# Performance work log

Hardware: AMD Instinct MI355X
Metric: run time of the kernel (lower is better)

Reference implementation:

```python
import jax, jax.numpy as jnp
import numpy as np

D_MODEL = 1024
D_STATE = 16
D_CONV = 4
EXPAND = 2
HEADDIM = 8
D_INNER = EXPAND * D_MODEL            # 2048
NHEADS = D_INNER // HEADDIM           # 256
CONV_DIM = D_INNER + 2 * D_STATE      # 2080 (ngroups=1)
D_IN_PROJ = 2 * D_INNER + 2 * D_STATE + NHEADS  # 4384
B_SZ, SEQ = 4, 2048
EPS = 1e-5


def setup_inputs() -> dict:
    key = jax.random.key(0)
    ks = jax.random.split(key, 8)
    return {
        "x": jax.random.normal(ks[0], (B_SZ, SEQ, D_MODEL), jnp.float32),
        "ln_w": jnp.ones((D_MODEL,), jnp.float32),
        "ln_b": jnp.zeros((D_MODEL,), jnp.float32),
        "W_in": jax.random.normal(ks[1], (D_MODEL, D_IN_PROJ), jnp.float32) * 0.02,
        "conv_w": jax.random.normal(ks[2], (D_CONV, 1, CONV_DIM), jnp.float32) * 0.2,
        "conv_b": jnp.zeros((CONV_DIM,), jnp.float32),
        "A_log": jnp.log(jax.random.uniform(ks[3], (NHEADS,), jnp.float32, 1.0, 16.0)),
        "Dp": jnp.ones((NHEADS,), jnp.float32) + 0.1 * jax.random.normal(ks[4], (NHEADS,), jnp.float32),
        "dt_bias": 0.5 * jax.random.normal(ks[5], (NHEADS,), jnp.float32),
        "rms_w": jnp.ones((D_INNER,), jnp.float32),
        "W_out": jax.random.normal(ks[6], (D_INNER, D_MODEL), jnp.float32) * 0.02,
    }


def _mamba_block(x, ln_w, ln_b, W_in, conv_w, conv_b, A_log, Dp, dt_bias, rms_w, W_out):
    B, L, _ = x.shape
    # pre-norm LayerNorm
    mu = jnp.mean(x, axis=-1, keepdims=True)
    var = jnp.mean((x - mu) ** 2, axis=-1, keepdims=True)
    xn = (x - mu) * jax.lax.rsqrt(var + EPS) * ln_w + ln_b

    # in_proj -> z, xBC, dt
    u = xn @ W_in                                    # (B, L, 4384)
    z = u[..., :D_INNER]
    xBC = u[..., D_INNER:D_INNER + CONV_DIM]
    dt = jax.nn.softplus(u[..., -NHEADS:] + dt_bias)  # (B, L, NHEADS)

    # causal depthwise conv1d + SiLU
    xp = jnp.pad(xBC, ((0, 0), (D_CONV - 1, 0), (0, 0)))
    xBC = jax.lax.conv_general_dilated(
        xp, conv_w, window_strides=(1,), padding="VALID",
        dimension_numbers=("NWC", "WIO", "NWC"), feature_group_count=CONV_DIM)
    xBC = jax.nn.silu(xBC + conv_b)

    xs = xBC[..., :D_INNER].reshape(B, L, NHEADS, HEADDIM)   # SSM input
    Bm = xBC[..., D_INNER:D_INNER + D_STATE]                  # (B, L, N)
    Cm = xBC[..., D_INNER + D_STATE:]                          # (B, L, N)

    A = -jnp.exp(A_log)                                       # (NHEADS,)

    def step(h, inp):
        # h: (B, H, P, N)
        x_t, B_t, C_t, dt_t = inp
        dA = jnp.exp(dt_t * A)                                 # (B, H)
        h = h * dA[..., None, None] + jnp.einsum("bh,bhp,bn->bhpn", dt_t, x_t, B_t)
        y = jnp.einsum("bhpn,bn->bhp", h, C_t)
        return h, y

    h0 = jnp.zeros((B, NHEADS, HEADDIM, D_STATE), x.dtype)
    _, ys = jax.lax.scan(step, h0, (xs.swapaxes(0, 1), Bm.swapaxes(0, 1),
                                     Cm.swapaxes(0, 1), dt.swapaxes(0, 1)))
    y = ys.swapaxes(0, 1) + Dp[None, None, :, None] * xs       # (B, L, H, P)
    y = y.reshape(B, L, D_INNER)

    # gated RMSNorm: rmsnorm(y * silu(z)) * weight
    g = y * jax.nn.silu(z)
    g = g * jax.lax.rsqrt(jnp.mean(g * g, axis=-1, keepdims=True) + EPS) * rms_w

    return x + g @ W_out


def reference(x, ln_w, ln_b, W_in, conv_w, conv_b, A_log, Dp, dt_bias, rms_w, W_out):
    return _mamba_block(x, ln_w, ln_b, W_in, conv_w, conv_b, A_log, Dp, dt_bias, rms_w, W_out)
```

## Files before the change

### kernel.cpp

```cpp
#include <hip/hip_runtime.h>

typedef __bf16 bf16;
typedef __attribute__((ext_vector_type(8))) __bf16 bf16x8;
typedef __attribute__((ext_vector_type(4))) float f32x4;

#define B_SZ 4
#define SEQ 2048
#define DM 1024
#define DIN 2048
#define NH 256
#define DSTATE 16
#define CONVD 2080
#define DPROJ 4384
#define NPAD1 4608
#define MROWS 8192
#define NC 64
#define LC 32
#define UROWB 8768

__device__ __forceinline__ void gload_lds16(const void* g, void* l) {
  __builtin_amdgcn_global_load_lds(
      (__attribute__((address_space(1))) void*)g,
      (__attribute__((address_space(3))) void*)l, 16, 0, 0);
}

template <int N>
__device__ __forceinline__ void vm_wait() {
  asm volatile("s_waitcnt vmcnt(%0)" ::"n"(N) : "memory");
}
__device__ __forceinline__ void bar() { asm volatile("s_barrier" ::: "memory"); }
__device__ __forceinline__ void lgkm0() {
  asm volatile("s_waitcnt lgkmcnt(0)" ::: "memory");
}

__global__ void transpose_cvt(const float* __restrict__ W, bf16* __restrict__ WT,
                              int K, int N, int Npad) {
  __shared__ float tile[32][33];
  int k0 = blockIdx.x * 32, n0 = blockIdx.y * 32;
  int tx = threadIdx.x, ty = threadIdx.y;
#pragma unroll
  for (int j = 0; j < 4; j++) {
    int k = k0 + ty + 8 * j, n = n0 + tx;
    tile[ty + 8 * j][tx] = (k < K && n < N) ? W[(size_t)k * N + n] : 0.f;
  }
  __syncthreads();
#pragma unroll
  for (int j = 0; j < 4; j++) {
    int n = n0 + ty + 8 * j, k = k0 + tx;
    if (n < Npad && k < K) WT[(size_t)n * K + k] = (bf16)tile[tx][ty + 8 * j];
  }
}

__global__ __launch_bounds__(256) void ln_kernel(const float* __restrict__ x,
                                                 const float* __restrict__ lw,
                                                 const float* __restrict__ lb,
                                                 bf16* __restrict__ xn) {
  int row = blockIdx.x;
  int t = threadIdx.x;
  f32x4 v4 = ((const f32x4*)(x + (size_t)row * DM))[t];
  float v0 = v4[0], v1 = v4[1], v2 = v4[2], v3 = v4[3];
  float s = v0 + v1 + v2 + v3;
  float s2 = v0 * v0 + v1 * v1 + v2 * v2 + v3 * v3;
#pragma unroll
  for (int off = 32; off > 0; off >>= 1) {
    s += __shfl_down(s, off);
    s2 += __shfl_down(s2, off);
  }
  __shared__ float ps[8];
  int wave = t >> 6, lane = t & 63;
  if (lane == 0) { ps[wave] = s; ps[4 + wave] = s2; }
  __syncthreads();
  s = ps[0] + ps[1] + ps[2] + ps[3];
  s2 = ps[4] + ps[5] + ps[6] + ps[7];
  float mean = s * (1.f / DM);
  float var = s2 * (1.f / DM) - mean * mean;
  float rstd = rsqrtf(var + 1e-5f);
  f32x4 wv = ((const f32x4*)lw)[t];
  f32x4 bv = ((const f32x4*)lb)[t];
  bf16 o[4];
  o[0] = (bf16)((v0 - mean) * rstd * wv[0] + bv[0]);
  o[1] = (bf16)((v1 - mean) * rstd * wv[1] + bv[1]);
  o[2] = (bf16)((v2 - mean) * rstd * wv[2] + bv[2]);
  o[3] = (bf16)((v3 - mean) * rstd * wv[3] + bv[3]);
  bf16* dst = xn + (size_t)row * DM + t * 4;
  dst[0] = o[0]; dst[1] = o[1]; dst[2] = o[2]; dst[3] = o[3];
}

#define G1_PHASE(MQ, NQ, P, STAGE, VMW)                                                    \
  {                                                                                        \
    const char* sa_ = lds + ((P) * 2 + (MQ)) * 16384;                                      \
    const char* sb_ = lds + 65536 + ((P) * 2 + (NQ)) * 16384;                              \
    bf16x8 a_[4][2], b_[2][2];                                                             \
    _Pragma("unroll") for (int mi = 0; mi < 4; mi++) {                                     \
      int lrow = wm * 64 + mi * 16 + lr16;                                                 \
      a_[mi][0] = *(const bf16x8*)(sa_ + lrow * 128 + ts0 * 16);                           \
      a_[mi][1] = *(const bf16x8*)(sa_ + lrow * 128 + ts1 * 16);                           \
    }                                                                                      \
    _Pragma("unroll") for (int ni = 0; ni < 2; ni++) {                                     \
      int lrow = wn * 32 + ni * 16 + lr16;                                                 \
      b_[ni][0] = *(const bf16x8*)(sb_ + lrow * 128 + ts0 * 16);                           \
      b_[ni][1] = *(const bf16x8*)(sb_ + lrow * 128 + ts1 * 16);                           \
    }                                                                                      \
    STAGE;                                                                                 \
    VMW;                                                                                   \
    bar();                                                                                 \
    lgkm0();                                                                               \
    __builtin_amdgcn_s_setprio(1);                                                         \
    _Pragma("unroll") for (int mi = 0; mi < 4; mi++)                                       \
      _Pragma("unroll") for (int ni = 0; ni < 2; ni++) {                                   \
        acc[(MQ) * 4 + mi][(NQ) * 2 + ni] = __builtin_amdgcn_mfma_f32_16x16x32_bf16(       \
            a_[mi][0], b_[ni][0], acc[(MQ) * 4 + mi][(NQ) * 2 + ni], 0, 0, 0);             \
        acc[(MQ) * 4 + mi][(NQ) * 2 + ni] = __builtin_amdgcn_mfma_f32_16x16x32_bf16(       \
            a_[mi][1], b_[ni][1], acc[(MQ) * 4 + mi][(NQ) * 2 + ni], 0, 0, 0);             \
      }                                                                                    \
    __builtin_amdgcn_s_setprio(0);                                                         \
    bar();                                                                                 \
  }

__global__ __launch_bounds__(512, 2) void gemm1_8p(const bf16* __restrict__ A,
                                                   const bf16* __restrict__ BT,
                                                   bf16* __restrict__ C) {
  __shared__ char lds[131072];
  int bid = blockIdx.x;
  int swz = (bid & 7) * 72 + (bid >> 3);
  int bm = swz / 18, bn = swz - (swz / 18) * 18;
  int m0 = bm * 256, n0 = bn * 256;
  int t = threadIdx.x, lane = t & 63, wave = t >> 6;
  int wm = wave >> 2, wn = wave & 3;
  int lr16 = lane & 15, kq = lane >> 4;
  int ts0 = kq ^ (lr16 & 7);
  int ts1 = (4 + kq) ^ (lr16 & 7);
  int sw = (lane & 7) ^ ((lane >> 3) & 7);
  int l8 = lane >> 3;
  int c0 = 2 * wave, c1 = 2 * wave + 1;
  int lr0 = c0 * 8 + l8, lr1 = c1 * 8 + l8;
  const char* Ab = (const char*)A;
  const char* Bb = (const char*)BT;
  int grA0 = m0 + (lr0 >> 6) * 128 + (lr0 & 63);
  int grA1 = m0 + (lr1 >> 6) * 128 + (lr1 & 63);
  int gcB0 = n0 + (lr0 >> 5) * 64 + (lr0 & 31);
  int gcB1 = n0 + (lr1 >> 5) * 64 + (lr1 & 31);

  auto stA = [&](int kt, int p, int mq) {
    char* slot = lds + (p * 2 + mq) * 16384;
    size_t ko = (size_t)kt * 128 + sw * 16;
    gload_lds16(Ab + (size_t)(grA0 + mq * 64) * 2048 + ko, slot + c0 * 1024);
    gload_lds16(Ab + (size_t)(grA1 + mq * 64) * 2048 + ko, slot + c1 * 1024);
  };
  auto stB = [&](int kt, int p, int nq) {
    char* slot = lds + 65536 + (p * 2 + nq) * 16384;
    size_t ko = (size_t)kt * 128 + sw * 16;
    gload_lds16(Bb + (size_t)(gcB0 + nq * 32) * 2048 + ko, slot + c0 * 1024);
    gload_lds16(Bb + (size_t)(gcB1 + nq * 32) * 2048 + ko, slot + c1 * 1024);
  };

  f32x4 acc[8][4] = {};
  stA(0, 0, 0); stB(0, 0, 0); stA(0, 0, 1); stB(0, 0, 1); stA(1, 1, 0); stB(1, 1, 0);
  vm_wait<8>();
  bar();
#pragma unroll 1
  for (int kt = 0; kt < 16; kt++) {
    int p = kt & 1;
    G1_PHASE(0, 0, p, { if (kt + 1 < 16) stA(kt + 1, p ^ 1, 1); },
             { if (kt < 15) vm_wait<6>(); else vm_wait<0>(); });
    G1_PHASE(0, 1, p, { if (kt + 1 < 16) stB(kt + 1, p ^ 1, 1); }, {});
    G1_PHASE(1, 0, p, { if (kt + 2 < 16) stA(kt + 2, p, 0); }, {});
    G1_PHASE(1, 1, p, { if (kt + 2 < 16) stB(kt + 2, p, 0); },
             { if (kt < 14) vm_wait<8>(); else if (kt == 14) vm_wait<4>(); });
  }
#pragma unroll
  for (int mq = 0; mq < 2; mq++)
#pragma unroll
    for (int mi = 0; mi < 4; mi++)
#pragma unroll
      for (int nq = 0; nq < 2; nq++)
#pragma unroll
        for (int ni = 0; ni < 2; ni++) {
          int row = m0 + wm * 128 + mq * 64 + mi * 16 + kq * 4;
          int col = n0 + wn * 64 + nq * 32 + ni * 16 + lr16;
          f32x4 v = acc[mq * 4 + mi][nq * 2 + ni];
          if (col < 4384) {
#pragma unroll
            for (int r = 0; r < 4; r++)
              C[(size_t)(row + r) * DPROJ + col] = (bf16)v[r];
          }
        }
}

#define G2_PHASE(MQ, P, STAGE, VMW)                                                        \
  {                                                                                        \
    const char* sa_ = lds + ((P) * 2 + (MQ)) * 16384;                                      \
    const char* sb_ = lds + 65536 + (P) * 16384;                                           \
    bf16x8 a_[4][2], b_[2][2];                                                             \
    _Pragma("unroll") for (int mi = 0; mi < 4; mi++) {                                     \
      int lrow = wm * 64 + mi * 16 + lr16;                                                 \
      a_[mi][0] = *(const bf16x8*)(sa_ + lrow * 128 + ts0 * 16);                           \
      a_[mi][1] = *(const bf16x8*)(sa_ + lrow * 128 + ts1 * 16);                           \
    }                                                                                      \
    _Pragma("unroll") for (int ni = 0; ni < 2; ni++) {                                     \
      int lrow = wn * 32 + ni * 16 + lr16;                                                 \
      b_[ni][0] = *(const bf16x8*)(sb_ + lrow * 128 + ts0 * 16);                           \
      b_[ni][1] = *(const bf16x8*)(sb_ + lrow * 128 + ts1 * 16);                           \
    }                                                                                      \
    STAGE;                                                                                 \
    VMW;                                                                                   \
    bar();                                                                                 \
    lgkm0();                                                                               \
    __builtin_amdgcn_s_setprio(1);                                                         \
    _Pragma("unroll") for (int mi = 0; mi < 4; mi++)                                       \
      _Pragma("unroll") for (int ni = 0; ni < 2; ni++) {                                   \
        acc[(MQ) * 4 + mi][ni] = __builtin_amdgcn_mfma_f32_16x16x32_bf16(                  \
            a_[mi][0], b_[ni][0], acc[(MQ) * 4 + mi][ni], 0, 0, 0);                        \
        acc[(MQ) * 4 + mi][ni] = __builtin_amdgcn_mfma_f32_16x16x32_bf16(                  \
            a_[mi][1], b_[ni][1], acc[(MQ) * 4 + mi][ni], 0, 0, 0);                        \
      }                                                                                    \
    __builtin_amdgcn_s_setprio(0);                                                         \
    bar();                                                                                 \
  }

__global__ __launch_bounds__(512, 2) void gemm2_8p(const bf16* __restrict__ A,
                                                   const bf16* __restrict__ BT,
                                                   float* __restrict__ C,
                                                   const float* __restrict__ Xres) {
  __shared__ char lds[98304];
  int bid = blockIdx.x;
  int swz = (bid & 7) * 32 + (bid >> 3);
  int bm = swz >> 3, bn = swz & 7;
  int m0 = bm * 256, n0 = bn * 128;
  int t = threadIdx.x, lane = t & 63, wave = t >> 6;
  int wm = wave >> 2, wn = wave & 3;
  int lr16 = lane & 15, kq = lane >> 4;
  int ts0 = kq ^ (lr16 & 7);
  int ts1 = (4 + kq) ^ (lr16 & 7);
  int sw = (lane & 7) ^ ((lane >> 3) & 7);
  int l8 = lane >> 3;
  int c0 = 2 * wave, c1 = 2 * wave + 1;
  int lr0 = c0 * 8 + l8, lr1 = c1 * 8 + l8;
  const char* Ab = (const char*)A;
  const char* Bb = (const char*)BT;
  int grA0 = m0 + (lr0 >> 6) * 128 + (lr0 & 63);
  int grA1 = m0 + (lr1 >> 6) * 128 + (lr1 & 63);
  int gcB0 = n0 + lr0, gcB1 = n0 + lr1;

  auto stA = [&](int kt, int p, int mq) {
    char* slot = lds + (p * 2 + mq) * 16384;
    size_t ko = (size_t)kt * 128 + sw * 16;
    gload_lds16(Ab + (size_t)(grA0 + mq * 64) * 4096 + ko, slot + c0 * 1024);
    gload_lds16(Ab + (size_t)(grA1 + mq * 64) * 4096 + ko, slot + c1 * 1024);
  };
  auto stB = [&](int kt, int p) {
    char* slot = lds + 65536 + p * 16384;
    size_t ko = (size_t)kt * 128 + sw * 16;
    gload_lds16(Bb + (size_t)gcB0 * 4096 + ko, slot + c0 * 1024);
    gload_lds16(Bb + (size_t)gcB1 * 4096 + ko, slot + c1 * 1024);
  };

  f32x4 acc[8][2] = {};
  stA(0, 0, 0); stB(0, 0); stA(0, 0, 1); stA(1, 1, 0);
  vm_wait<4>();
  bar();
#pragma unroll 1
  for (int kt = 0; kt < 32; kt++) {
    int p = kt & 1;
    G2_PHASE(0, p, { if (kt + 1 < 32) { stB(kt + 1, p ^ 1); stA(kt + 1, p ^ 1, 1); } },
             { if (kt < 31) vm_wait<6>(); else vm_wait<0>(); });
    G2_PHASE(1, p, { if (kt + 2 < 32) stA(kt + 2, p, 0); },
             { if (kt < 30) vm_wait<4>(); else if (kt == 30) vm_wait<2>(); });
  }
#pragma unroll
  for (int mq = 0; mq < 2; mq++)
#pragma unroll
    for (int mi = 0; mi < 4; mi++)
#pragma unroll
      for (int ni = 0; ni < 2; ni++) {
        int row = m0 + wm * 128 + mq * 64 + mi * 16 + kq * 4;
        int col = n0 + wn * 32 + ni * 16 + lr16;
        f32x4 v = acc[mq * 4 + mi][ni];
#pragma unroll
        for (int r = 0; r < 4; r++) {
          size_t o = (size_t)(row + r) * DM + col;
          C[o] = Xres[o] + v[r];
        }
      }
}

__global__ __launch_bounds__(256) void conv_prep3(const bf16* __restrict__ u,
                                                  const float* __restrict__ cw,
                                                  const float* __restrict__ cb,
                                                  const float* __restrict__ dt_bias,
                                                  bf16* __restrict__ xs,
                                                  float* __restrict__ BC,
                                                  float* __restrict__ dtf) {
  const int JPR = 292;
  int idx = blockIdx.x * 256 + threadIdx.x;
  if (idx >= MROWS * JPR) return;
  int row = idx / JPR;
  int j = idx - row * JPR;
  int t = row & (SEQ - 1);
  if (j < 260) {
    int c0 = j * 8;
    float acc[8];
#pragma unroll
    for (int i = 0; i < 8; i++) acc[i] = cb[c0 + i];
    const bf16* ub = u + (size_t)row * DPROJ + DIN + c0;
#pragma unroll
    for (int tap = 0; tap < 4; tap++) {
      int tt = t - 3 + tap;
      if (tt >= 0) {
        bf16x8 uv = *(const bf16x8*)(ub + (ptrdiff_t)(tap - 3) * DPROJ);
        const float* wv = cw + tap * CONVD + c0;
#pragma unroll
        for (int i = 0; i < 8; i++) acc[i] += wv[i] * (float)uv[i];
      }
    }
    if (c0 < DIN) {
      bf16x8 o;
#pragma unroll
      for (int i = 0; i < 8; i++) {
        float sv = acc[i] / (1.f + __expf(-acc[i]));
        o[i] = (bf16)sv;
      }
      *(bf16x8*)(xs + (size_t)row * DIN + c0) = o;
    } else {
      float* bc = BC + (size_t)row * 32 + (c0 - DIN);
#pragma unroll
      for (int i = 0; i < 8; i++) bc[i] = acc[i] / (1.f + __expf(-acc[i]));
    }
  } else {
    int h0 = (j - 260) * 8;
    bf16x8 uv = *(const bf16x8*)(u + (size_t)row * DPROJ + (DPROJ - NH) + h0);
    float* dst = dtf + (size_t)row * NH + h0;
#pragma unroll
    for (int i = 0; i < 8; i++) {
      float xv = (float)uv[i] + dt_bias[h0 + i];
      dst[i] = (xv > 20.f) ? xv : log1pf(__expf(xv));
    }
  }
}

__global__ __launch_bounds__(64) void scan_p1(const bf16* __restrict__ xs,
                                              const float* __restrict__ BC,
                                              const float* __restrict__ dtf,
                                              const float* __restrict__ A_log,
                                              bf16* __restrict__ uscr) {
  int c = blockIdx.x & 63, hg = (blockIdx.x >> 6) & 31, b = blockIdx.x >> 11;
  int lane = threadIdx.x, hh = lane >> 3;
  int h = hg * 8 + hh;
  float A = -__expf(A_log[h]);
  float st[16];
#pragma unroll
  for (int n = 0; n < 16; n++) st[n] = 0.f;
  float pcum = 1.f;
  size_t rb = (size_t)b * SEQ + (size_t)c * LC;
  for (int t = 0; t < LC; t++) {
    size_t row = rb + t;
    const float* bcrow = BC + row * 32;
    float dtv = dtf[row * NH + h];
    float x = (float)xs[row * DIN + hg * 64 + lane];
    float dA = __expf(dtv * A);
    pcum *= dA;
    float w = dtv * x;
#pragma unroll
    for (int n = 0; n < 16; n++) st[n] = st[n] * dA + w * bcrow[n];
  }
  char* slot = (char*)uscr + (size_t)blockIdx.x * UROWB + 4096;
  float* S = (float*)slot;
#pragma unroll
  for (int n = 0; n < 16; n++) S[lane * 16 + n] = st[n];
  if ((lane & 7) == 0) ((float*)(slot + 4096))[hh] = pcum;
}

__global__ __launch_bounds__(64) void scan_p2(bf16* __restrict__ uscr) {
  int bh = blockIdx.x;
  int lane = threadIdx.x, hh = lane >> 3;
  float H[16];
#pragma unroll
  for (int n = 0; n < 16; n++) H[n] = 0.f;
  char* base = (char*)uscr + (size_t)bh * NC * UROWB + 4096;
  float sN[16], PN;
  {
    float* S = (float*)base;
#pragma unroll
    for (int n = 0; n < 16; n++) sN[n] = S[lane * 16 + n];
    PN = ((const float*)(base + 4096))[hh];
  }
  for (int c = 0; c < NC; c++) {
    float sC[16], PC = PN;
#pragma unroll
    for (int n = 0; n < 16; n++) sC[n] = sN[n];
    if (c + 1 < NC) {
      char* slot = base + (size_t)(c + 1) * UROWB;
      float* S = (float*)slot;
#pragma unroll
      for (int n = 0; n < 16; n++) sN[n] = S[lane * 16 + n];
      PN = ((const float*)(slot + 4096))[hh];
    }
    float* S0 = (float*)(base + (size_t)c * UROWB);
#pragma unroll
    for (int n = 0; n < 16; n++) {
      float hn = H[n];
      S0[lane * 16 + n] = hn;
      H[n] = PC * hn + sC[n];
    }
  }
}

__global__ __launch_bounds__(64) void scan_p3(const bf16* __restrict__ xs,
                                              const float* __restrict__ BC,
                                              const float* __restrict__ dtf,
                                              const float* __restrict__ A_log,
                                              const float* __restrict__ Dp,
                                              const bf16* __restrict__ uscr,
                                              bf16* __restrict__ y) {
  int c = blockIdx.x & 63, hg = (blockIdx.x >> 6) & 31, b = blockIdx.x >> 11;
  int lane = threadIdx.x, hh = lane >> 3;
  int h = hg * 8 + hh;
  float A = -__expf(A_log[h]);
  float D = Dp[h];
  const char* slot = (const char*)uscr + (size_t)blockIdx.x * UROWB + 4096;
  float st[16];
#pragma unroll
  for (int n = 0; n < 16; n++) st[n] = ((const float*)slot)[lane * 16 + n];
  size_t rb = (size_t)b * SEQ + (size_t)c * LC;
  for (int t = 0; t < LC; t++) {
    size_t row = rb + t;
    const float* bcrow = BC + row * 32;
    float dtv = dtf[row * NH + h];
    float x = (float)xs[row * DIN + hg * 64 + lane];
    float dA = __expf(dtv * A);
    float w = dtv * x;
    float yv = 0.f;
#pragma unroll
    for (int n = 0; n < 16; n++) {
      st[n] = st[n] * dA + w * bcrow[n];
      yv += st[n] * bcrow[16 + n];
    }
    y[row * DIN + hg * 64 + lane] = (bf16)(yv + D * x);
  }
}

__global__ __launch_bounds__(256) void gate_rms(const bf16* __restrict__ u,
                                                const bf16* __restrict__ y,
                                                const float* __restrict__ rms_w,
                                                bf16* __restrict__ g) {
  int row = blockIdx.x;
  int t = threadIdx.x;
  bf16x8 zv = ((const bf16x8*)(u + (size_t)row * DPROJ))[t];
  bf16x8 yv = ((const bf16x8*)(y + (size_t)row * DIN))[t];
  float gv[8];
  float s2 = 0.f;
#pragma unroll
  for (int i = 0; i < 8; i++) {
    float z = (float)zv[i];
    float yy = (float)yv[i];
    float gg = yy * z / (1.f + __expf(-z));
    gv[i] = gg;
    s2 += gg * gg;
  }
#pragma unroll
  for (int off = 32; off > 0; off >>= 1) s2 += __shfl_down(s2, off);
  __shared__ float ps[4];
  int wave = t >> 6, lane = t & 63;
  if (lane == 0) ps[wave] = s2;
  __syncthreads();
  s2 = ps[0] + ps[1] + ps[2] + ps[3];
  float scale = rsqrtf(s2 * (1.f / DIN) + 1e-5f);
  f32x4 w0 = ((const f32x4*)rms_w)[2 * t];
  f32x4 w1 = ((const f32x4*)rms_w)[2 * t + 1];
  bf16x8 og;
#pragma unroll
  for (int i = 0; i < 4; i++) og[i] = (bf16)(gv[i] * scale * w0[i]);
#pragma unroll
  for (int i = 0; i < 4; i++) og[4 + i] = (bf16)(gv[4 + i] * scale * w1[i]);
  ((bf16x8*)(g + (size_t)row * DIN))[t] = og;
}

extern "C" void kernel_launch(void* const* d_in, const int* in_sizes, int n_in,
                              void* d_out, int out_size, void* d_ws, size_t ws_size,
                              hipStream_t stream) {
  const float* x = (const float*)d_in[0];
  const float* lnw = (const float*)d_in[1];
  const float* lnb = (const float*)d_in[2];
  const float* Win = (const float*)d_in[3];
  const float* cw = (const float*)d_in[4];
  const float* cb = (const float*)d_in[5];
  const float* Alog = (const float*)d_in[6];
  const float* Dpv = (const float*)d_in[7];
  const float* dtb = (const float*)d_in[8];
  const float* rmsw = (const float*)d_in[9];
  const float* Wout = (const float*)d_in[10];
  float* out = (float*)d_out;

  char* ws = (char*)d_ws;
  bf16* u = (bf16*)(ws + 0);
  bf16* xnb = (bf16*)(ws + 71827456);
  bf16* WinT = (bf16*)(ws + 88604672);
  bf16* yb = (bf16*)(ws + 71827456);
  bf16* xsb = (bf16*)(ws + 105381888);
  bf16* gb = (bf16*)(ws + 105381888);
  float* BC = (float*)(ws + 138936320);
  float* dtf = (float*)(ws + 139984896);
  bf16* WoutT = (bf16*)(ws + 148373504);

  transpose_cvt<<<dim3(32, 144), dim3(32, 8), 0, stream>>>(Win, WinT, 1024, DPROJ, NPAD1);
  transpose_cvt<<<dim3(64, 32), dim3(32, 8), 0, stream>>>(Wout, WoutT, DIN, DM, DM);
  ln_kernel<<<MROWS, 256, 0, stream>>>(x, lnw, lnb, xnb);
  gemm1_8p<<<576, 512, 0, stream>>>(xnb, WinT, u);
  conv_prep3<<<(MROWS * 292) / 256, 256, 0, stream>>>(u, cw, cb, dtb, xsb, BC, dtf);
  scan_p1<<<MROWS, 64, 0, stream>>>(xsb, BC, dtf, Alog, u);
  scan_p2<<<128, 64, 0, stream>>>(u);
  scan_p3<<<MROWS, 64, 0, stream>>>(xsb, BC, dtf, Alog, Dpv, u, yb);
  gate_rms<<<MROWS, 256, 0, stream>>>(u, yb, rmsw, gb);
  gemm2_8p<<<256, 512, 0, stream>>>(gb, WoutT, out, x);
}
```

Before: 321.5 us.

## Restructure in_proj GEMM main loop into two phases with full-width B fragments

Rewrites the gemm1 k-loop from four quarter-tile phases into two half-tile phases. Each phase loads all four B fragments once and reuses them across both A halves, and B is staged as one 256-column slab per buffer. This halves the barriers per k-step and reduces repeated LDS reads of B. The cost is more live registers for B fragments and a rebalanced global-load wait schedule, which could hurt occupancy or overlap.

```diff
diff --git a/kernel.cpp b/kernel.cpp
--- a/kernel.cpp
+++ b/kernel.cpp
@@ -86,37 +86,6 @@
   dst[0] = o[0]; dst[1] = o[1]; dst[2] = o[2]; dst[3] = o[3];
 }
 
-#define G1_PHASE(MQ, NQ, P, STAGE, VMW)                                                    \
-  {                                                                                        \
-    const char* sa_ = lds + ((P) * 2 + (MQ)) * 16384;                                      \
-    const char* sb_ = lds + 65536 + ((P) * 2 + (NQ)) * 16384;                              \
-    bf16x8 a_[4][2], b_[2][2];                                                             \
-    _Pragma("unroll") for (int mi = 0; mi < 4; mi++) {                                     \
-      int lrow = wm * 64 + mi * 16 + lr16;                                                 \
-      a_[mi][0] = *(const bf16x8*)(sa_ + lrow * 128 + ts0 * 16);                           \
-      a_[mi][1] = *(const bf16x8*)(sa_ + lrow * 128 + ts1 * 16);                           \
-    }                                                                                      \
-    _Pragma("unroll") for (int ni = 0; ni < 2; ni++) {                                     \
-      int lrow = wn * 32 + ni * 16 + lr16;                                                 \
-      b_[ni][0] = *(const bf16x8*)(sb_ + lrow * 128 + ts0 * 16);                           \
-      b_[ni][1] = *(const bf16x8*)(sb_ + lrow * 128 + ts1 * 16);                           \
-    }                                                                                      \
-    STAGE;                                                                                 \
-    VMW;                                                                                   \
-    bar();                                                                                 \
-    lgkm0();                                                                               \
-    __builtin_amdgcn_s_setprio(1);                                                         \
-    _Pragma("unroll") for (int mi = 0; mi < 4; mi++)                                       \
-      _Pragma("unroll") for (int ni = 0; ni < 2; ni++) {                                   \
-        acc[(MQ) * 4 + mi][(NQ) * 2 + ni] = __builtin_amdgcn_mfma_f32_16x16x32_bf16(       \
-            a_[mi][0], b_[ni][0], acc[(MQ) * 4 + mi][(NQ) * 2 + ni], 0, 0, 0);             \
-        acc[(MQ) * 4 + mi][(NQ) * 2 + ni] = __builtin_amdgcn_mfma_f32_16x16x32_bf16(       \
-            a_[mi][1], b_[ni][1], acc[(MQ) * 4 + mi][(NQ) * 2 + ni], 0, 0, 0);             \
-      }                                                                                    \
-    __builtin_amdgcn_s_setprio(0);                                                         \
-    bar();                                                                                 \
-  }
-
 __global__ __launch_bounds__(512, 2) void gemm1_8p(const bf16* __restrict__ A,
                                                    const bf16* __restrict__ BT,
                                                    bf16* __restrict__ C) {
@@ -130,61 +99,111 @@
   int lr16 = lane & 15, kq = lane >> 4;
   int ts0 = kq ^ (lr16 & 7);
   int ts1 = (4 + kq) ^ (lr16 & 7);
-  int sw = (lane & 7) ^ ((lane >> 3) & 7);
+  int sw = (lane & 7) ^ (lane >> 3);
   int l8 = lane >> 3;
-  int c0 = 2 * wave, c1 = 2 * wave + 1;
-  int lr0 = c0 * 8 + l8, lr1 = c1 * 8 + l8;
   const char* Ab = (const char*)A;
   const char* Bb = (const char*)BT;
-  int grA0 = m0 + (lr0 >> 6) * 128 + (lr0 & 63);
-  int grA1 = m0 + (lr1 >> 6) * 128 + (lr1 & 63);
-  int gcB0 = n0 + (lr0 >> 5) * 64 + (lr0 & 31);
-  int gcB1 = n0 + (lr1 >> 5) * 64 + (lr1 & 31);
-
-  auto stA = [&](int kt, int p, int mq) {
-    char* slot = lds + (p * 2 + mq) * 16384;
+
+  auto stA = [&](int kt, int p, int h) {
+    char* slot = lds + (p * 2 + h) * 16384;
     size_t ko = (size_t)kt * 128 + sw * 16;
-    gload_lds16(Ab + (size_t)(grA0 + mq * 64) * 2048 + ko, slot + c0 * 1024);
-    gload_lds16(Ab + (size_t)(grA1 + mq * 64) * 2048 + ko, slot + c1 * 1024);
+#pragma unroll
+    for (int g = 0; g < 2; g++) {
+      int c = wave * 2 + g;
+      int L = c * 8 + l8;
+      int grow = m0 + ((L >> 6) << 7) + h * 64 + (L & 63);
+      gload_lds16(Ab + (size_t)grow * 2048 + ko, slot + c * 1024);
+    }
   };
-  auto stB = [&](int kt, int p, int nq) {
-    char* slot = lds + 65536 + (p * 2 + nq) * 16384;
+  auto stB = [&](int kt, int p) {
+    char* slot = lds + 65536 + p * 32768;
     size_t ko = (size_t)kt * 128 + sw * 16;
-    gload_lds16(Bb + (size_t)(gcB0 + nq * 32) * 2048 + ko, slot + c0 * 1024);
-    gload_lds16(Bb + (size_t)(gcB1 + nq * 32) * 2048 + ko, slot + c1 * 1024);
+#pragma unroll
+    for (int g = 0; g < 4; g++) {
+      int c = wave * 4 + g;
+      gload_lds16(Bb + (size_t)(n0 + c * 8 + l8) * 2048 + ko, slot + c * 1024);
+    }
   };
 
   f32x4 acc[8][4] = {};
-  stA(0, 0, 0); stB(0, 0, 0); stA(0, 0, 1); stB(0, 0, 1); stA(1, 1, 0); stB(1, 1, 0);
-  vm_wait<8>();
+  bf16x8 b_[4][2];
+  stA(0, 0, 0); stB(0, 0); stA(0, 0, 1); stA(1, 1, 0); stB(1, 1);
+  vm_wait<6>();
   bar();
 #pragma unroll 1
   for (int kt = 0; kt < 16; kt++) {
     int p = kt & 1;
-    G1_PHASE(0, 0, p, { if (kt + 1 < 16) stA(kt + 1, p ^ 1, 1); },
-             { if (kt < 15) vm_wait<6>(); else vm_wait<0>(); });
-    G1_PHASE(0, 1, p, { if (kt + 1 < 16) stB(kt + 1, p ^ 1, 1); }, {});
-    G1_PHASE(1, 0, p, { if (kt + 2 < 16) stA(kt + 2, p, 0); }, {});
-    G1_PHASE(1, 1, p, { if (kt + 2 < 16) stB(kt + 2, p, 0); },
-             { if (kt < 14) vm_wait<8>(); else if (kt == 14) vm_wait<4>(); });
+    {
+      const char* sa_ = lds + (p * 2 + 0) * 16384;
+      const char* sb_ = lds + 65536 + p * 32768;
+      bf16x8 a_[4][2];
+#pragma unroll
+      for (int mi = 0; mi < 4; mi++) {
+        int lrow = wm * 64 + mi * 16 + lr16;
+        a_[mi][0] = *(const bf16x8*)(sa_ + lrow * 128 + ts0 * 16);
+        a_[mi][1] = *(const bf16x8*)(sa_ + lrow * 128 + ts1 * 16);
+      }
+#pragma unroll
+      for (int ni = 0; ni < 4; ni++) {
+        int lrow = wn * 64 + ni * 16 + lr16;
+        b_[ni][0] = *(const bf16x8*)(sb_ + lrow * 128 + ts0 * 16);
+        b_[ni][1] = *(const bf16x8*)(sb_ + lrow * 128 + ts1 * 16);
+      }
+      if (kt < 15) stA(kt + 1, p ^ 1, 1);
+      if (kt < 15) vm_wait<8>(); else vm_wait<0>();
+      bar();
+      lgkm0();
+      __builtin_amdgcn_s_setprio(1);
+#pragma unroll
+      for (int mi = 0; mi < 4; mi++)
+#pragma unroll
+        for (int ni = 0; ni < 4; ni++) {
+          acc[mi][ni] = __builtin_amdgcn_mfma_f32_16x16x32_bf16(a_[mi][0], b_[ni][0], acc[mi][ni], 0, 0, 0);
+          acc[mi][ni] = __builtin_amdgcn_mfma_f32_16x16x32_bf16(a_[mi][1], b_[ni][1], acc[mi][ni], 0, 0, 0);
+        }
+      __builtin_amdgcn_s_setprio(0);
+      bar();
+    }
+    {
+      const char* sa_ = lds + (p * 2 + 1) * 16384;
+      bf16x8 a_[4][2];
+#pragma unroll
+      for (int mi = 0; mi < 4; mi++) {
+        int lrow = wm * 64 + mi * 16 + lr16;
+        a_[mi][0] = *(const bf16x8*)(sa_ + lrow * 128 + ts0 * 16);
+        a_[mi][1] = *(const bf16x8*)(sa_ + lrow * 128 + ts1 * 16);
+      }
+      if (kt < 14) { stA(kt + 2, p, 0); stB(kt + 2, p); }
+      if (kt < 14) vm_wait<8>(); else if (kt == 14) vm_wait<2>();
+      bar();
+      lgkm0();
+      __builtin_amdgcn_s_setprio(1);
+#pragma unroll
+      for (int mi = 0; mi < 4; mi++)
+#pragma unroll
+        for (int ni = 0; ni < 4; ni++) {
+          acc[4 + mi][ni] = __builtin_amdgcn_mfma_f32_16x16x32_bf16(a_[mi][0], b_[ni][0], acc[4 + mi][ni], 0, 0, 0);
+          acc[4 + mi][ni] = __builtin_amdgcn_mfma_f32_16x16x32_bf16(a_[mi][1], b_[ni][1], acc[4 + mi][ni], 0, 0, 0);
+        }
+      __builtin_amdgcn_s_setprio(0);
+      bar();
+    }
   }
 #pragma unroll
   for (int mq = 0; mq < 2; mq++)
 #pragma unroll
     for (int mi = 0; mi < 4; mi++)
 #pragma unroll
-      for (int nq = 0; nq < 2; nq++)
-#pragma unroll
-        for (int ni = 0; ni < 2; ni++) {
-          int row = m0 + wm * 128 + mq * 64 + mi * 16 + kq * 4;
-          int col = n0 + wn * 64 + nq * 32 + ni * 16 + lr16;
-          f32x4 v = acc[mq * 4 + mi][nq * 2 + ni];
-          if (col < 4384) {
-#pragma unroll
-            for (int r = 0; r < 4; r++)
-              C[(size_t)(row + r) * DPROJ + col] = (bf16)v[r];
-          }
+      for (int ni = 0; ni < 4; ni++) {
+        int row = m0 + wm * 128 + mq * 64 + mi * 16 + kq * 4;
+        int col = n0 + wn * 64 + ni * 16 + lr16;
+        f32x4 v = acc[mq * 4 + mi][ni];
+        if (col < 4384) {
+#pragma unroll
+          for (int r = 0; r < 4; r++)
+            C[(size_t)(row + r) * DPROJ + col] = (bf16)v[r];
         }
+      }
 }
 
 #define G2_PHASE(MQ, P, STAGE, VMW)                                                        \
```

After: 311.6 us. -3.1%, faster.

## Restructure in-proj GEMM LDS layout and reuse fragment registers across phases

Applied to the files above, without the earlier changes.

Rewrites the 256x256 in-projection GEMM main loop so the A and B tiles sit in LDS as contiguous per-wave halves rather than interleaved quarter slots. The loop is unrolled over two k-tiles into eight phases that keep A and B fragments in registers (aL/aH, b01/b23) and reload only what changed, roughly halving LDS reads per MFMA. The prefetch schedule and vmcnt waits are reordered to match. The more irregular staging order risks exposing load latency or getting the wait counts wrong.

```diff
diff --git a/kernel.cpp b/kernel.cpp
--- a/kernel.cpp
+++ b/kernel.cpp
@@ -86,32 +86,35 @@
   dst[0] = o[0]; dst[1] = o[1]; dst[2] = o[2]; dst[3] = o[3];
 }
 
-#define G1_PHASE(MQ, NQ, P, STAGE, VMW)                                                    \
+#define G1PH(RDA, AARR, RDB, BARR, MQ, NQ, P, STAGE, WAIT)                                 \
   {                                                                                        \
-    const char* sa_ = lds + ((P) * 2 + (MQ)) * 16384;                                      \
-    const char* sb_ = lds + 65536 + ((P) * 2 + (NQ)) * 16384;                              \
-    bf16x8 a_[4][2], b_[2][2];                                                             \
-    _Pragma("unroll") for (int mi = 0; mi < 4; mi++) {                                     \
-      int lrow = wm * 64 + mi * 16 + lr16;                                                 \
-      a_[mi][0] = *(const bf16x8*)(sa_ + lrow * 128 + ts0 * 16);                           \
-      a_[mi][1] = *(const bf16x8*)(sa_ + lrow * 128 + ts1 * 16);                           \
+    const char* sa_ = lds + (P) * 32768 + wm * 16384;                                      \
+    const char* sb_ = lds + 65536 + (P) * 32768 + (wn >> 1) * 16384;                       \
+    if (RDA) {                                                                             \
+      _Pragma("unroll") for (int mi = 0; mi < 4; mi++) {                                   \
+        int lrow = ((MQ) * 4 + mi) * 16 + lr16;                                            \
+        AARR[mi][0] = *(const bf16x8*)(sa_ + lrow * 128 + ts0 * 16);                       \
+        AARR[mi][1] = *(const bf16x8*)(sa_ + lrow * 128 + ts1 * 16);                       \
+      }                                                                                    \
     }                                                                                      \
-    _Pragma("unroll") for (int ni = 0; ni < 2; ni++) {                                     \
-      int lrow = wn * 32 + ni * 16 + lr16;                                                 \
-      b_[ni][0] = *(const bf16x8*)(sb_ + lrow * 128 + ts0 * 16);                           \
-      b_[ni][1] = *(const bf16x8*)(sb_ + lrow * 128 + ts1 * 16);                           \
+    if (RDB) {                                                                             \
+      _Pragma("unroll") for (int ni = 0; ni < 2; ni++) {                                   \
+        int lrow = (wn & 1) * 64 + ((NQ) * 2 + ni) * 16 + lr16;                            \
+        BARR[ni][0] = *(const bf16x8*)(sb_ + lrow * 128 + ts0 * 16);                       \
+        BARR[ni][1] = *(const bf16x8*)(sb_ + lrow * 128 + ts1 * 16);                       \
+      }                                                                                    \
     }                                                                                      \
     STAGE;                                                                                 \
-    VMW;                                                                                   \
+    WAIT;                                                                                  \
     bar();                                                                                 \
     lgkm0();                                                                               \
     __builtin_amdgcn_s_setprio(1);                                                         \
     _Pragma("unroll") for (int mi = 0; mi < 4; mi++)                                       \
       _Pragma("unroll") for (int ni = 0; ni < 2; ni++) {                                   \
         acc[(MQ) * 4 + mi][(NQ) * 2 + ni] = __builtin_amdgcn_mfma_f32_16x16x32_bf16(       \
-            a_[mi][0], b_[ni][0], acc[(MQ) * 4 + mi][(NQ) * 2 + ni], 0, 0, 0);             \
+            AARR[mi][0], BARR[ni][0], acc[(MQ) * 4 + mi][(NQ) * 2 + ni], 0, 0, 0);         \
         acc[(MQ) * 4 + mi][(NQ) * 2 + ni] = __builtin_amdgcn_mfma_f32_16x16x32_bf16(       \
-            a_[mi][1], b_[ni][1], acc[(MQ) * 4 + mi][(NQ) * 2 + ni], 0, 0, 0);             \
+            AARR[mi][1], BARR[ni][1], acc[(MQ) * 4 + mi][(NQ) * 2 + ni], 0, 0, 0);         \
       }                                                                                    \
     __builtin_amdgcn_s_setprio(0);                                                         \
     bar();                                                                                 \
@@ -130,61 +133,67 @@
   int lr16 = lane & 15, kq = lane >> 4;
   int ts0 = kq ^ (lr16 & 7);
   int ts1 = (4 + kq) ^ (lr16 & 7);
-  int sw = (lane & 7) ^ ((lane >> 3) & 7);
+  int sw = (lane & 7) ^ (lane >> 3);
   int l8 = lane >> 3;
-  int c0 = 2 * wave, c1 = 2 * wave + 1;
-  int lr0 = c0 * 8 + l8, lr1 = c1 * 8 + l8;
   const char* Ab = (const char*)A;
   const char* Bb = (const char*)BT;
-  int grA0 = m0 + (lr0 >> 6) * 128 + (lr0 & 63);
-  int grA1 = m0 + (lr1 >> 6) * 128 + (lr1 & 63);
-  int gcB0 = n0 + (lr0 >> 5) * 64 + (lr0 & 31);
-  int gcB1 = n0 + (lr1 >> 5) * 64 + (lr1 & 31);
-
-  auto stA = [&](int kt, int p, int mq) {
-    char* slot = lds + (p * 2 + mq) * 16384;
+
+  auto stA = [&](int kt, int p, int h) {
+    char* slot = lds + p * 32768 + h * 16384;
     size_t ko = (size_t)kt * 128 + sw * 16;
-    gload_lds16(Ab + (size_t)(grA0 + mq * 64) * 2048 + ko, slot + c0 * 1024);
-    gload_lds16(Ab + (size_t)(grA1 + mq * 64) * 2048 + ko, slot + c1 * 1024);
+#pragma unroll
+    for (int g = 0; g < 2; g++) {
+      int c = wave * 2 + g;
+      gload_lds16(Ab + (size_t)(m0 + h * 128 + c * 8 + l8) * 2048 + ko, slot + c * 1024);
+    }
   };
-  auto stB = [&](int kt, int p, int nq) {
-    char* slot = lds + 65536 + (p * 2 + nq) * 16384;
+  auto stB = [&](int kt, int p, int h) {
+    char* slot = lds + 65536 + p * 32768 + h * 16384;
     size_t ko = (size_t)kt * 128 + sw * 16;
-    gload_lds16(Bb + (size_t)(gcB0 + nq * 32) * 2048 + ko, slot + c0 * 1024);
-    gload_lds16(Bb + (size_t)(gcB1 + nq * 32) * 2048 + ko, slot + c1 * 1024);
+#pragma unroll
+    for (int g = 0; g < 2; g++) {
+      int c = wave * 2 + g;
+      gload_lds16(Bb + (size_t)(n0 + h * 128 + c * 8 + l8) * 2048 + ko, slot + c * 1024);
+    }
   };
 
   f32x4 acc[8][4] = {};
-  stA(0, 0, 0); stB(0, 0, 0); stA(0, 0, 1); stB(0, 0, 1); stA(1, 1, 0); stB(1, 1, 0);
-  vm_wait<8>();
+  bf16x8 aL[4][2], aH[4][2], b01[2][2], b23[2][2];
+
+  stA(0, 0, 0); stA(0, 0, 1); stB(0, 0, 0); stB(0, 0, 1);
+  stB(1, 1, 0); stB(1, 1, 1);
+  vm_wait<4>();
   bar();
 #pragma unroll 1
-  for (int kt = 0; kt < 16; kt++) {
-    int p = kt & 1;
-    G1_PHASE(0, 0, p, { if (kt + 1 < 16) stA(kt + 1, p ^ 1, 1); },
-             { if (kt < 15) vm_wait<6>(); else vm_wait<0>(); });
-    G1_PHASE(0, 1, p, { if (kt + 1 < 16) stB(kt + 1, p ^ 1, 1); }, {});
-    G1_PHASE(1, 0, p, { if (kt + 2 < 16) stA(kt + 2, p, 0); }, {});
-    G1_PHASE(1, 1, p, { if (kt + 2 < 16) stB(kt + 2, p, 0); },
-             { if (kt < 14) vm_wait<8>(); else if (kt == 14) vm_wait<4>(); });
+  for (int it = 0; it < 8; ++it) {
+    int e2 = 2 * it + 2, o1 = 2 * it + 1, o3 = 2 * it + 3;
+    bool st = it < 7;
+    G1PH(1, aL, 1, b01, 0, 0, 0, { stA(o1, 1, 0); }, {});
+    G1PH(0, aL, 1, b23, 0, 1, 0, { stA(o1, 1, 1); }, {});
+    G1PH(1, aH, 0, b01, 1, 0, 0, { if (st) stB(e2, 0, 0); }, {});
+    G1PH(0, aH, 0, b23, 1, 1, 0, { if (st) stB(e2, 0, 1); },
+         { if (st) vm_wait<4>(); else vm_wait<0>(); });
+    G1PH(1, aL, 1, b01, 0, 0, 1, { if (st) stA(e2, 0, 0); }, {});
+    G1PH(0, aL, 1, b23, 0, 1, 1, { if (st) stA(e2, 0, 1); }, {});
+    G1PH(1, aH, 0, b01, 1, 0, 1, { if (st) stB(o3, 1, 0); }, {});
+    G1PH(0, aH, 0, b23, 1, 1, 1, { if (st) stB(o3, 1, 1); },
+         { if (st) vm_wait<4>(); });
   }
 #pragma unroll
   for (int mq = 0; mq < 2; mq++)
 #pragma unroll
     for (int mi = 0; mi < 4; mi++)
 #pragma unroll
-      for (int nq = 0; nq < 2; nq++)
-#pragma unroll
-        for (int ni = 0; ni < 2; ni++) {
-          int row = m0 + wm * 128 + mq * 64 + mi * 16 + kq * 4;
-          int col = n0 + wn * 64 + nq * 32 + ni * 16 + lr16;
-          f32x4 v = acc[mq * 4 + mi][nq * 2 + ni];
-          if (col < 4384) {
-#pragma unroll
-            for (int r = 0; r < 4; r++)
-              C[(size_t)(row + r) * DPROJ + col] = (bf16)v[r];
-          }
+      for (int ni = 0; ni < 4; ni++) {
+        int row = m0 + wm * 128 + (mq * 4 + mi) * 16 + kq * 4;
+        int col = n0 + wn * 64 + ni * 16 + lr16;
+        f32x4 v = acc[mq * 4 + mi][ni];
+        if (col < 4384) {
+#pragma unroll
+          for (int r = 0; r < 4; r++)
+            C[(size_t)(row + r) * DPROJ + col] = (bf16)v[r];
         }
+      }
 }
 
 #define G2_PHASE(MQ, P, STAGE, VMW)                                                        \
```

Measured after the change: 303.4 us. 5.6% less time.
